# Kernel tuning notes

Measured on AMD Instinct MI355X. Metric: run time of the kernel, lower is better.

## Reference

```python
import jax, jax.numpy as jnp
import numpy as np

N = 8192
IN_FEATS = 512
OUT_FEATS = 512


def setup_inputs() -> dict:
    key = jax.random.key(0)
    k_adj, k_feat, k_w = jax.random.split(key, 3)
    adj = jax.random.uniform(k_adj, (N, N), dtype=jnp.float32)
    features = jax.random.normal(k_feat, (N, IN_FEATS), dtype=jnp.float32)
    # nn.Linear(in_feats, out_feats, bias=False): weight is [out, in]; we store transposed [in, out]
    W = jax.random.normal(k_w, (IN_FEATS, OUT_FEATS), dtype=jnp.float32) / np.sqrt(IN_FEATS)
    return {"adj": adj, "features": features, "W": W}


def reference(adj, features, W):
    n = adj.shape[0]
    # adj + I (self loops)
    a = adj + jnp.eye(n, dtype=adj.dtype)
    # symmetric degree normalization D^{-1/2} A D^{-1/2}
    deg = jnp.sum(a, axis=1)  # [N]
    d_inv_sqrt = jnp.where(deg > 0, jax.lax.rsqrt(deg), 0.0)  # inf -> 0 as in torch code
    # diag(d) @ a @ diag(d) == d[:,None] * a * d[None,:] (algebraic simplification of O(N^3) diag matmuls)
    norm_adj = d_inv_sqrt[:, None] * a * d_inv_sqrt[None, :]  # [N, N]
    h = norm_adj @ features  # [N, in]
    return h @ W  # [N, out]
```

## Files before the change

### kernel.cpp

```cpp
#include <hip/hip_runtime.h>
#include <cstdint>
#include <cstddef>

#define NN 8192
#define NF 512

typedef __attribute__((ext_vector_type(8))) short bf16x8;
typedef __attribute__((ext_vector_type(4))) float f32x4;

__device__ __forceinline__ unsigned short f2bf_bits(float f) {
  unsigned u = __builtin_bit_cast(unsigned, f);
  u += 0x7FFFu + ((u >> 16) & 1u);
  return (unsigned short)(u >> 16);
}

__device__ __forceinline__ bf16x8 cvt8(float4 a, float4 b) {
  bf16x8 r;
  r[0] = (short)f2bf_bits(a.x); r[1] = (short)f2bf_bits(a.y);
  r[2] = (short)f2bf_bits(a.z); r[3] = (short)f2bf_bits(a.w);
  r[4] = (short)f2bf_bits(b.x); r[5] = (short)f2bf_bits(b.y);
  r[6] = (short)f2bf_bits(b.z); r[7] = (short)f2bf_bits(b.w);
  return r;
}

__device__ __forceinline__ void gld_lds16(const void* g, void* l) {
  __builtin_amdgcn_global_load_lds(
      (const __attribute__((address_space(1))) unsigned int*)g,
      (__attribute__((address_space(3))) unsigned int*)l, 16, 0, 0);
}

template <bool CVT>
__global__ void k_rowsum(const float* __restrict__ adj, float* __restrict__ dinv,
                         short* __restrict__ adjb) {
  const int row = blockIdx.x;
  const float4* p = (const float4*)(adj + (size_t)row * NN);
  short* ob = CVT ? (adjb + (size_t)row * NN) : nullptr;
  float s = 0.f;
#pragma unroll
  for (int j = 0; j < 8; ++j) {
    float4 v = p[j * 256 + threadIdx.x];
    s += (v.x + v.y) + (v.z + v.w);
    if (CVT) {
      ushort4 o;
      o.x = f2bf_bits(v.x); o.y = f2bf_bits(v.y);
      o.z = f2bf_bits(v.z); o.w = f2bf_bits(v.w);
      *(ushort4*)&ob[(size_t)(j * 256 + threadIdx.x) * 4] = o;
    }
  }
#pragma unroll
  for (int off = 32; off > 0; off >>= 1) s += __shfl_down(s, off, 64);
  __shared__ float red[4];
  if ((threadIdx.x & 63) == 0) red[threadIdx.x >> 6] = s;
  __syncthreads();
  if (threadIdx.x == 0) {
    float deg = red[0] + red[1] + red[2] + red[3] + 1.0f;
    dinv[row] = (deg > 0.f) ? (1.0f / sqrtf(deg)) : 0.f;
  }
}

template <bool SCALE>
__global__ void k_transpose(const float* __restrict__ src, int rows, int cols,
                            const float* __restrict__ dinv, short* __restrict__ dst) {
  __shared__ float tile[32][33];
  const int c0 = blockIdx.x * 32, r0 = blockIdx.y * 32;
  const int tx = threadIdx.x & 31, ty = threadIdx.x >> 5;
#pragma unroll
  for (int i = 0; i < 32; i += 8) {
    float v = src[(size_t)(r0 + ty + i) * cols + c0 + tx];
    if (SCALE) v *= dinv[r0 + ty + i];
    tile[ty + i][tx] = v;
  }
  __syncthreads();
#pragma unroll
  for (int i = 0; i < 32; i += 8)
    dst[(size_t)(c0 + ty + i) * rows + r0 + tx] = (short)f2bf_bits(tile[tx][ty + i]);
}

template <bool A_BF16, bool GCN_EPI>
__global__ __launch_bounds__(512, 2)
void k_gemm2(const void* __restrict__ Ap, const short* __restrict__ Bt,
             int N, int K,
             const float* __restrict__ dinv, const float* __restrict__ feat,
             void* __restrict__ Cp) {
  __shared__ __align__(16) short As[4][128 * 64];
  __shared__ __align__(16) short Bs[4][128 * 64];
  const int tid = threadIdx.x;
  const int lane = tid & 63;
  const int w = tid >> 6;
  const int wm = (w >> 1) & 1, wn = w & 1, kk = w >> 2;

  const int bid = blockIdx.y * gridDim.x + blockIdx.x;
  const int nb = gridDim.x * gridDim.y;
  const int sbid = ((nb & 7) == 0) ? ((bid & 7) * (nb >> 3) + (bid >> 3)) : bid;
  const int n0 = (sbid % gridDim.x) * 128;
  const int m0 = (sbid / gridDim.x) * 128;
  const int nt = K >> 6;

  f32x4 acc[4][4];
#pragma unroll
  for (int m = 0; m < 4; ++m)
#pragma unroll
    for (int n = 0; n < 4; ++n) acc[m][n] = (f32x4){0.f, 0.f, 0.f, 0.f};

  auto stage_b = [&](int buf, int t) {
    const int kofs = t << 6;
#pragma unroll
    for (int q = 0; q < 2; ++q) {
      const int rblk = (w << 4) + (q << 3);
      const int r = rblk + (lane >> 3);
      const int sc = (lane & 7) ^ (r & 7);
      gld_lds16(Bt + (size_t)(n0 + r) * K + kofs + (sc << 3), &Bs[buf][rblk << 6]);
    }
  };
  auto stage_a = [&](int buf, int t) {
    const int kofs = t << 6;
    if constexpr (A_BF16) {
      const short* Ab = (const short*)Ap;
#pragma unroll
      for (int q = 0; q < 2; ++q) {
        const int rblk = (w << 4) + (q << 3);
        const int r = rblk + (lane >> 3);
        const int sc = (lane & 7) ^ (r & 7);
        gld_lds16(Ab + (size_t)(m0 + r) * K + kofs + (sc << 3), &As[buf][rblk << 6]);
      }
    } else {
      const float* Af = (const float*)Ap;
      const int r = tid >> 2;
      const int c0 = (tid & 3) << 4;
      const float* s = Af + (size_t)(m0 + r) * K + kofs + c0;
      float4 x0 = ((const float4*)s)[0], x1 = ((const float4*)s)[1];
      float4 x2 = ((const float4*)s)[2], x3 = ((const float4*)s)[3];
      const int cc = (tid & 3) << 1;
      *(bf16x8*)&As[buf][(r << 6) + ((cc ^ (r & 7)) << 3)]       = cvt8(x0, x1);
      *(bf16x8*)&As[buf][(r << 6) + (((cc + 1) ^ (r & 7)) << 3)] = cvt8(x2, x3);
    }
  };
  auto compute = [&](int buf) {
    const int lr = lane & 15, kg = lane >> 4;
    const int lc = (kk << 2) + kg;
    bf16x8 a[4], b[4];
#pragma unroll
    for (int m = 0; m < 4; ++m) {
      const int r = (wm << 6) + (m << 4) + lr;
      a[m] = *(const bf16x8*)&As[buf][(r << 6) + ((lc ^ (r & 7)) << 3)];
    }
#pragma unroll
    for (int n = 0; n < 4; ++n) {
      const int r = (wn << 6) + (n << 4) + lr;
      b[n] = *(const bf16x8*)&Bs[buf][(r << 6) + ((lc ^ (r & 7)) << 3)];
    }
    __builtin_amdgcn_s_setprio(1);
#pragma unroll
    for (int m = 0; m < 4; ++m)
#pragma unroll
      for (int n = 0; n < 4; ++n)
        acc[m][n] = __builtin_amdgcn_mfma_f32_16x16x32_bf16(a[m], b[n], acc[m][n], 0, 0, 0);
    __builtin_amdgcn_s_setprio(0);
  };

  stage_a(0, 0); stage_b(0, 0);
  stage_a(1, 1); stage_b(1, 1);

  for (int t = 0; t < nt; ++t) {
    if (t + 2 < nt) { stage_a((t + 2) & 3, t + 2); stage_b((t + 2) & 3, t + 2); }
    if constexpr (A_BF16) {
      if (t + 2 < nt)      asm volatile("s_waitcnt vmcnt(8)" ::: "memory");
      else if (t + 1 < nt) asm volatile("s_waitcnt vmcnt(4)" ::: "memory");
      else                 asm volatile("s_waitcnt vmcnt(0)" ::: "memory");
      __builtin_amdgcn_s_barrier();
      __builtin_amdgcn_sched_barrier(0);
    } else {
      __syncthreads();
    }
    compute(t & 3);
  }

  __syncthreads();
  float* red = (float*)&As[0][0];
  if (w >= 4) {
    float* my = red + ((w - 4) << 12);
#pragma unroll
    for (int m = 0; m < 4; ++m)
#pragma unroll
      for (int n = 0; n < 4; ++n)
        *(f32x4*)&my[(((m << 2) + n) << 8) + (lane << 2)] = acc[m][n];
  }
  __syncthreads();
  if (w < 4) {
    float* my = red + (w << 12);
#pragma unroll
    for (int m = 0; m < 4; ++m)
#pragma unroll
      for (int n = 0; n < 4; ++n)
        acc[m][n] += *(const f32x4*)&my[(((m << 2) + n) << 8) + (lane << 2)];

    const int cl = lane & 15, rg = lane >> 4;
#pragma unroll
    for (int m = 0; m < 4; ++m) {
#pragma unroll
      for (int n = 0; n < 4; ++n) {
#pragma unroll
        for (int j = 0; j < 4; ++j) {
          const int gi = m0 + (wm << 6) + (m << 4) + (rg << 2) + j;
          const int gn = n0 + (wn << 6) + (n << 4) + cl;
          const float v = acc[m][n][j];
          if constexpr (GCN_EPI) {
            const float d = dinv[gi];
            const float hv = d * v + d * d * feat[(size_t)gi * NF + gn];
            ((unsigned short*)Cp)[(size_t)gi * N + gn] = f2bf_bits(hv);
          } else {
            ((float*)Cp)[(size_t)gi * N + gn] = v;
          }
        }
      }
    }
  }
}

extern "C" void kernel_launch(void* const* d_in, const int* in_sizes, int n_in,
                              void* d_out, int out_size, void* d_ws, size_t ws_size,
                              hipStream_t stream) {
  const float* adj  = (const float*)d_in[0];
  const float* feat = (const float*)d_in[1];
  const float* W    = (const float*)d_in[2];

  char* ws = (char*)d_ws;
  float* dinv = (float*)ws;
  short* FbT  = (short*)(ws + 32768);
  short* WbT  = (short*)(ws + 32768 + 8388608);
  short* Hb   = (short*)(ws + 32768 + 8388608 + 524288);
  short* adjb = (short*)(ws + 32768 + 8388608 + 524288 + 8388608);
  float* out  = (float*)d_out;
  const bool big_ws = ws_size >= (size_t)(32768 + 8388608 + 524288 + 8388608) +
                                 (size_t)NN * NN * 2;

  if (big_ws) {
    k_rowsum<true><<<NN, 256, 0, stream>>>(adj, dinv, adjb);
  } else {
    k_rowsum<false><<<NN, 256, 0, stream>>>(adj, dinv, nullptr);
  }
  k_transpose<true ><<<dim3(NF / 32, NN / 32), 256, 0, stream>>>(feat, NN, NF, dinv, FbT);
  k_transpose<false><<<dim3(NF / 32, NF / 32), 256, 0, stream>>>(W, NF, NF, nullptr, WbT);

  if (big_ws) {
    k_gemm2<true, true ><<<dim3(NF / 128, NN / 128), 512, 0, stream>>>(
        adjb, FbT, NF, NN, dinv, feat, Hb);
  } else {
    k_gemm2<false, true ><<<dim3(NF / 128, NN / 128), 512, 0, stream>>>(
        adj, FbT, NF, NN, dinv, feat, Hb);
  }
  k_gemm2<true, false><<<dim3(NF / 128, NN / 128), 512, 0, stream>>>(
      Hb, WbT, NF, NF, nullptr, nullptr, out);
}
```

Before: 207.6 us.

## Interleave LDS reads, global prefetch and MFMA halves in GEMM main loop

Restructures the bf16 GEMM main loop into two half-phases. Each half issues its LDS fragment reads and part of the next-tile global-to-LDS prefetch, then runs eight MFMAs, with explicit barriers and waitcnts placed between phases. The aim is to hide LDS read latency and spread global load issue across the MFMA stream rather than stalling before a single compute block. The finer-grained manual scheduling adds barrier points and relies on hand-set vmcnt values, which risks stalls or correctness problems if the counts are off.

```diff
diff --git a/kernel.cpp b/kernel.cpp
--- a/kernel.cpp
+++ b/kernel.cpp
@@ -102,6 +102,9 @@
 #pragma unroll
     for (int n = 0; n < 4; ++n) acc[m][n] = (f32x4){0.f, 0.f, 0.f, 0.f};
 
+  const int lr = lane & 15, kg = lane >> 4;
+  const int lc = (kk << 2) + kg;
+
   auto stage_b = [&](int buf, int t) {
     const int kofs = t << 6;
 #pragma unroll
@@ -114,65 +117,99 @@
   };
   auto stage_a = [&](int buf, int t) {
     const int kofs = t << 6;
-    if constexpr (A_BF16) {
-      const short* Ab = (const short*)Ap;
-#pragma unroll
-      for (int q = 0; q < 2; ++q) {
-        const int rblk = (w << 4) + (q << 3);
-        const int r = rblk + (lane >> 3);
-        const int sc = (lane & 7) ^ (r & 7);
-        gld_lds16(Ab + (size_t)(m0 + r) * K + kofs + (sc << 3), &As[buf][rblk << 6]);
-      }
-    } else {
-      const float* Af = (const float*)Ap;
-      const int r = tid >> 2;
-      const int c0 = (tid & 3) << 4;
-      const float* s = Af + (size_t)(m0 + r) * K + kofs + c0;
-      float4 x0 = ((const float4*)s)[0], x1 = ((const float4*)s)[1];
-      float4 x2 = ((const float4*)s)[2], x3 = ((const float4*)s)[3];
-      const int cc = (tid & 3) << 1;
-      *(bf16x8*)&As[buf][(r << 6) + ((cc ^ (r & 7)) << 3)]       = cvt8(x0, x1);
-      *(bf16x8*)&As[buf][(r << 6) + (((cc + 1) ^ (r & 7)) << 3)] = cvt8(x2, x3);
-    }
-  };
-  auto compute = [&](int buf) {
-    const int lr = lane & 15, kg = lane >> 4;
-    const int lc = (kk << 2) + kg;
-    bf16x8 a[4], b[4];
+    const short* Ab = (const short*)Ap;
+#pragma unroll
+    for (int q = 0; q < 2; ++q) {
+      const int rblk = (w << 4) + (q << 3);
+      const int r = rblk + (lane >> 3);
+      const int sc = (lane & 7) ^ (r & 7);
+      gld_lds16(Ab + (size_t)(m0 + r) * K + kofs + (sc << 3), &As[buf][rblk << 6]);
+    }
+  };
+  auto stage_a_f32 = [&](int buf, int t) {
+    const int kofs = t << 6;
+    const float* Af = (const float*)Ap;
+    const int r = tid >> 2;
+    const int c0 = (tid & 3) << 4;
+    const float* s = Af + (size_t)(m0 + r) * K + kofs + c0;
+    float4 x0 = ((const float4*)s)[0], x1 = ((const float4*)s)[1];
+    float4 x2 = ((const float4*)s)[2], x3 = ((const float4*)s)[3];
+    const int cc = (tid & 3) << 1;
+    *(bf16x8*)&As[buf][(r << 6) + ((cc ^ (r & 7)) << 3)]       = cvt8(x0, x1);
+    *(bf16x8*)&As[buf][(r << 6) + (((cc + 1) ^ (r & 7)) << 3)] = cvt8(x2, x3);
+  };
+
+  auto read_a = [&](int buf, bf16x8* a) {
 #pragma unroll
     for (int m = 0; m < 4; ++m) {
       const int r = (wm << 6) + (m << 4) + lr;
       a[m] = *(const bf16x8*)&As[buf][(r << 6) + ((lc ^ (r & 7)) << 3)];
     }
-#pragma unroll
-    for (int n = 0; n < 4; ++n) {
-      const int r = (wn << 6) + (n << 4) + lr;
-      b[n] = *(const bf16x8*)&Bs[buf][(r << 6) + ((lc ^ (r & 7)) << 3)];
-    }
-    __builtin_amdgcn_s_setprio(1);
+  };
+  auto read_b2 = [&](int buf, int nh, bf16x8* b) {
+#pragma unroll
+    for (int i = 0; i < 2; ++i) {
+      const int r = (wn << 6) + (((nh << 1) + i) << 4) + lr;
+      b[i] = *(const bf16x8*)&Bs[buf][(r << 6) + ((lc ^ (r & 7)) << 3)];
+    }
+  };
+  auto mfma8 = [&](bf16x8* a, bf16x8* b, int nh) {
 #pragma unroll
     for (int m = 0; m < 4; ++m)
 #pragma unroll
-      for (int n = 0; n < 4; ++n)
-        acc[m][n] = __builtin_amdgcn_mfma_f32_16x16x32_bf16(a[m], b[n], acc[m][n], 0, 0, 0);
-    __builtin_amdgcn_s_setprio(0);
-  };
-
-  stage_a(0, 0); stage_b(0, 0);
-  stage_a(1, 1); stage_b(1, 1);
-
-  for (int t = 0; t < nt; ++t) {
-    if (t + 2 < nt) { stage_a((t + 2) & 3, t + 2); stage_b((t + 2) & 3, t + 2); }
-    if constexpr (A_BF16) {
-      if (t + 2 < nt)      asm volatile("s_waitcnt vmcnt(8)" ::: "memory");
-      else if (t + 1 < nt) asm volatile("s_waitcnt vmcnt(4)" ::: "memory");
-      else                 asm volatile("s_waitcnt vmcnt(0)" ::: "memory");
+      for (int i = 0; i < 2; ++i)
+        acc[m][(nh << 1) + i] =
+            __builtin_amdgcn_mfma_f32_16x16x32_bf16(a[m], b[i], acc[m][(nh << 1) + i], 0, 0, 0);
+  };
+
+  if constexpr (A_BF16) {
+    stage_a(0, 0); stage_b(0, 0);
+    stage_a(1, 1); stage_b(1, 1);
+    asm volatile("s_waitcnt vmcnt(4)" ::: "memory");
+    __builtin_amdgcn_s_barrier();
+    __builtin_amdgcn_sched_barrier(0);
+
+    for (int t = 0; t < nt; ++t) {
+      const int cur = t & 3;
+      const bool more = (t + 2 < nt);
+      bf16x8 a[4], b0[2], b1[2];
+      read_a(cur, a);
+      read_b2(cur, 0, b0);
+      if (more) stage_a((t + 2) & 3, t + 2);
       __builtin_amdgcn_s_barrier();
-      __builtin_amdgcn_sched_barrier(0);
-    } else {
+      asm volatile("s_waitcnt lgkmcnt(0)" ::: "memory");
+      __builtin_amdgcn_sched_barrier(0);
+      __builtin_amdgcn_s_setprio(1);
+      mfma8(a, b0, 0);
+      __builtin_amdgcn_s_setprio(0);
+      __builtin_amdgcn_sched_barrier(0);
+      read_b2(cur, 1, b1);
+      if (more) stage_b((t + 2) & 3, t + 2);
+      asm volatile("s_waitcnt lgkmcnt(0)" ::: "memory");
+      __builtin_amdgcn_sched_barrier(0);
+      __builtin_amdgcn_s_setprio(1);
+      mfma8(a, b1, 1);
+      __builtin_amdgcn_s_setprio(0);
+      __builtin_amdgcn_sched_barrier(0);
+      if (more)                asm volatile("s_waitcnt vmcnt(4)" ::: "memory");
+      else if (t + 1 < nt)     asm volatile("s_waitcnt vmcnt(0)" ::: "memory");
+      __builtin_amdgcn_s_barrier();
+      __builtin_amdgcn_sched_barrier(0);
+    }
+  } else {
+    stage_a_f32(0, 0); stage_b(0, 0);
+    stage_a_f32(1, 1); stage_b(1, 1);
+    __syncthreads();
+    for (int t = 0; t < nt; ++t) {
+      const int cur = t & 3;
+      if (t + 2 < nt) { stage_a_f32((t + 2) & 3, t + 2); stage_b((t + 2) & 3, t + 2); }
+      bf16x8 a[4], b0[2], b1[2];
+      read_a(cur, a); read_b2(cur, 0, b0); read_b2(cur, 1, b1);
+      __builtin_amdgcn_s_setprio(1);
+      mfma8(a, b0, 0); mfma8(a, b1, 1);
+      __builtin_amdgcn_s_setprio(0);
       __syncthreads();
     }
-    compute(t & 3);
   }
 
   __syncthreads();
```

Measured after the change: 205.1 us. No clear change (-1.2%).
